# Kernel tuning notes

Hardware: AMD Instinct MI355X
Metric: run time of the kernel (lower is better)

Reference implementation:

```python
import jax, jax.numpy as jnp
import numpy as np

N_EMBED = 1024
N_HEAD = 16
HEAD_SIZE = N_EMBED // N_HEAD
LN_EPS = 1e-5


def setup_inputs() -> dict:
    key = jax.random.key(0)
    ks = jax.random.split(key, 12)
    B, T, C = 8, 1024, N_EMBED
    s = 0.02
    return {
        "x": jax.random.normal(ks[0], (B, T, C), dtype=jnp.float32),
        "Wq": jax.random.normal(ks[1], (C, C), dtype=jnp.float32) * s,
        "Wk": jax.random.normal(ks[2], (C, C), dtype=jnp.float32) * s,
        "Wv": jax.random.normal(ks[3], (C, C), dtype=jnp.float32) * s,
        "Wp": jax.random.normal(ks[4], (C, C), dtype=jnp.float32) * s,
        "bp": jnp.zeros((C,), dtype=jnp.float32),
        "ln1_g": jnp.ones((C,), dtype=jnp.float32),
        "ln1_b": jnp.zeros((C,), dtype=jnp.float32),
        "ln2_g": jnp.ones((C,), dtype=jnp.float32),
        "ln2_b": jnp.zeros((C,), dtype=jnp.float32),
        "W1": jax.random.normal(ks[5], (C, 4 * C), dtype=jnp.float32) * s,
        "b1": jnp.zeros((4 * C,), dtype=jnp.float32),
        "W2": jax.random.normal(ks[6], (4 * C, C), dtype=jnp.float32) * s,
        "b2": jnp.zeros((C,), dtype=jnp.float32),
    }


def _layernorm(x, g, b):
    mu = jnp.mean(x, axis=-1, keepdims=True)
    var = jnp.mean(jnp.square(x - mu), axis=-1, keepdims=True)
    return (x - mu) * jax.lax.rsqrt(var + LN_EPS) * g + b


def _block(x, Wq, Wk, Wv, Wp, bp, ln1_g, ln1_b, ln2_g, ln2_b, W1, b1, W2, b2):
    B, T, C = x.shape
    H, D = N_HEAD, HEAD_SIZE
    xn = _layernorm(x, ln1_g, ln1_b)
    # fused QKV for all heads (heads concatenated along feature dim, same as torch cat)
    q = (xn @ Wq).reshape(B, T, H, D)
    k = (xn @ Wk).reshape(B, T, H, D)
    v = (xn @ Wv).reshape(B, T, H, D)
    scores = jnp.einsum("bthd,bshd->bhts", q, k) / jnp.sqrt(jnp.float32(D))
    causal = jnp.tril(jnp.ones((T, T), dtype=bool))
    scores = jnp.where(causal, scores, jnp.float32(-jnp.inf))
    wei = jax.nn.softmax(scores, axis=-1)  # dropout = identity (eval)
    attn = jnp.einsum("bhts,bshd->bthd", wei, v).reshape(B, T, C)
    sa_out = attn @ Wp + bp  # dropout = identity (eval)
    x = x + sa_out
    xn2 = _layernorm(x, ln2_g, ln2_b)
    ff = jax.nn.relu(xn2 @ W1 + b1) @ W2 + b2  # dropout = identity (eval)
    return x + ff


def reference(x, Wq, Wk, Wv, Wp, bp, ln1_g, ln1_b, ln2_g, ln2_b, W1, b1, W2, b2):
    return _block(x, Wq, Wk, Wv, Wp, bp, ln1_g, ln1_b, ln2_g, ln2_b, W1, b1, W2, b2)
```

## Files before the change

kernel.cpp:

```cpp
#include <hip/hip_runtime.h>
#include <cstdint>
#include <cstddef>

using u16 = unsigned short;
typedef __attribute__((ext_vector_type(8))) short bh8;
typedef __attribute__((ext_vector_type(4))) float f4;

__device__ __forceinline__ u16 f2bf(float f) {
    union { float f; uint32_t u; } c; c.f = f;
    uint32_t u = c.u;
    u += 0x7FFFu + ((u >> 16) & 1u);
    return (u16)(u >> 16);
}

__device__ __forceinline__ void gload16(const void* g, void* l) {
    __builtin_amdgcn_global_load_lds(
        (__attribute__((address_space(1))) void*)g,
        (__attribute__((address_space(3))) void*)l,
        16, 0, 0);
}

__device__ __forceinline__ f4 mfma16(bh8 a, bh8 b, f4 c) {
    return __builtin_amdgcn_mfma_f32_16x16x32_bf16(a, b, c, 0, 0, 0);
}

__global__ __launch_bounds__(256) void wconv_kernel(
    const float* __restrict__ W, u16* __restrict__ Wt, int K, int N)
{
    __shared__ float t[32][33];
    const int tx = threadIdx.x & 31, ty = threadIdx.x >> 5;
    const int n0 = blockIdx.x * 32, k0 = blockIdx.y * 32;
#pragma unroll
    for (int j = 0; j < 4; ++j)
        t[ty + 8 * j][tx] = W[(size_t)(k0 + ty + 8 * j) * N + n0 + tx];
    __syncthreads();
#pragma unroll
    for (int j = 0; j < 4; ++j)
        Wt[(size_t)(n0 + ty + 8 * j) * K + k0 + tx] = f2bf(t[tx][ty + 8 * j]);
}

__global__ __launch_bounds__(256) void ln_kernel(
    const float* __restrict__ x, const float* __restrict__ g,
    const float* __restrict__ b, u16* __restrict__ out)
{
    const int row = blockIdx.x;
    const int tid = threadIdx.x;
    const float4 v = ((const float4*)(x + (size_t)row * 1024))[tid];
    float s  = v.x + v.y + v.z + v.w;
    float sq = v.x * v.x + v.y * v.y + v.z * v.z + v.w * v.w;
#pragma unroll
    for (int m = 1; m < 64; m <<= 1) {
        s  += __shfl_xor(s, m);
        sq += __shfl_xor(sq, m);
    }
    __shared__ float red[8];
    const int w = tid >> 6;
    if ((tid & 63) == 0) { red[w * 2] = s; red[w * 2 + 1] = sq; }
    __syncthreads();
    s  = red[0] + red[2] + red[4] + red[6];
    sq = red[1] + red[3] + red[5] + red[7];
    const float mu   = s * (1.0f / 1024.0f);
    const float var  = sq * (1.0f / 1024.0f) - mu * mu;
    const float rstd = rsqrtf(var + 1e-5f);
    const float4 gv = ((const float4*)g)[tid];
    const float4 bv = ((const float4*)b)[tid];
    ushort4 o;
    o.x = f2bf((v.x - mu) * rstd * gv.x + bv.x);
    o.y = f2bf((v.y - mu) * rstd * gv.y + bv.y);
    o.z = f2bf((v.z - mu) * rstd * gv.z + bv.z);
    o.w = f2bf((v.w - mu) * rstd * gv.w + bv.w);
    ((ushort4*)(out + (size_t)row * 1024))[tid] = o;
}

__global__ __launch_bounds__(256) void vtrans_kernel(
    const u16* __restrict__ vb, u16* __restrict__ vtb)
{
    __shared__ u16 t[64][66];
    const int bh = blockIdx.y;
    const int t0 = blockIdx.x * 64;
    const int b = bh >> 4, h = bh & 15;
    const u16* src = vb + (size_t)b * 1024 * 1024 + h * 64;
    const int rs = threadIdx.x >> 3, cs = threadIdx.x & 7;
#pragma unroll
    for (int it = 0; it < 2; ++it) {
        const int r = it * 32 + rs;
        *(uint4*)&t[r][cs * 8] = *(const uint4*)(src + (size_t)(t0 + r) * 1024 + cs * 8);
    }
    __syncthreads();
    u16* dst = vtb + (size_t)bh * 65536 + t0;
#pragma unroll
    for (int it = 0; it < 2; ++it) {
        const int d = it * 32 + rs;
        u16 tmp[8];
#pragma unroll
        for (int j = 0; j < 8; ++j) tmp[j] = t[cs * 8 + j][d];
        *(uint4*)(dst + (size_t)d * 1024 + cs * 8) = *(const uint4*)tmp;
    }
}

template <int NF, int EPI>
__global__ __launch_bounds__(512) void gemm8_kernel(
    const u16* __restrict__ A, const u16* __restrict__ Bt,
    int M, int N, int K, int KT,
    const float* __restrict__ bias, const float* __restrict__ resid,
    float* __restrict__ outf, u16* __restrict__ outb)
{
    constexpr int BN = NF * 64;
    __shared__ u16 Al[2][256 * 64];
    __shared__ u16 Bl[2][BN * 64];

    const int tid  = threadIdx.x;
    const int lane = tid & 63;
    const int w    = tid >> 6;
    const int wr   = w >> 2;
    const int wc   = w & 3;
    const int lrow = lane & 15;
    const int lg   = lane >> 4;

    const int gx  = gridDim.x, gy = gridDim.y;
    const int nwg = gx * gy * gridDim.z;
    const int lin = (blockIdx.z * gy + blockIdx.y) * gx + blockIdx.x;
    const int swz = (lin & 7) * (nwg >> 3) + (lin >> 3);
    const int nt  = swz % gx;
    const int tmq = swz / gx;
    const int mt  = tmq % gy;
    const int kz  = tmq / gy;
    const int kb  = kz * KT;

    auto stageA = [&](int slot, int h, int kt) {
#pragma unroll
        for (int it = 0; it < 2; ++it) {
            const int r = h * 128 + it * 64 + (tid >> 3);
            gload16(A + (size_t)(mt * 256 + r) * K + kt * 64 + (((tid & 7) ^ (r & 7)) << 3),
                    (char*)Al[slot] + (h * 128 + it * 64) * 128 + tid * 16);
        }
    };
    auto stageB = [&](int slot, int h, int kt) {
#pragma unroll
        for (int it = 0; it < NF / 2; ++it) {
            const int r = h * (BN / 2) + it * 64 + (tid >> 3);
            gload16(Bt + (size_t)(nt * BN + r) * K + kt * 64 + (((tid & 7) ^ (r & 7)) << 3),
                    (char*)Bl[slot] + (h * (BN / 2) + it * 64) * 128 + tid * 16);
        }
    };

    f4 acc[8][NF] = {};
    bh8 af[8];
    bh8 bf[NF];

    auto readFrags = [&](int slot, int ks) {
#pragma unroll
        for (int fm = 0; fm < 8; ++fm) {
            const int R = wr * 128 + fm * 16 + lrow;
            af[fm] = *(const bh8*)&Al[slot][R * 64 + ((((ks << 2) + lg) ^ (R & 7)) << 3)];
        }
#pragma unroll
        for (int fn = 0; fn < NF; ++fn) {
            const int R = wc * (NF * 16) + fn * 16 + lrow;
            bf[fn] = *(const bh8*)&Bl[slot][R * 64 + ((((ks << 2) + lg) ^ (R & 7)) << 3)];
        }
    };
    auto mfmaHalf = [&](int mh) {
#pragma unroll
        for (int fm = 0; fm < 4; ++fm)
#pragma unroll
            for (int fn = 0; fn < NF; ++fn)
                acc[mh * 4 + fm][fn] = mfma16(af[mh * 4 + fm], bf[fn], acc[mh * 4 + fm][fn]);
    };

    stageA(0, 0, kb); stageA(0, 1, kb); stageB(0, 0, kb); stageB(0, 1, kb);
    stageA(1, 0, kb + 1);
    asm volatile("s_waitcnt vmcnt(2)" ::: "memory");
    __builtin_amdgcn_s_barrier();
    __builtin_amdgcn_sched_barrier(0);

    auto doTile = [&](int t, int s, bool stN, bool stN2, bool g2) {
        readFrags(s, 0);
        if (stN) stageA(s ^ 1, 1, kb + t + 1);
        __builtin_amdgcn_s_barrier();
        asm volatile("s_waitcnt lgkmcnt(0)" ::: "memory");
        __builtin_amdgcn_sched_barrier(0);
        __builtin_amdgcn_s_setprio(1);
        mfmaHalf(0);
        __builtin_amdgcn_s_setprio(0);
        __builtin_amdgcn_s_barrier();
        __builtin_amdgcn_sched_barrier(0);
        if (stN) stageB(s ^ 1, 0, kb + t + 1);
        __builtin_amdgcn_s_barrier();
        __builtin_amdgcn_sched_barrier(0);
        __builtin_amdgcn_s_setprio(1);
        mfmaHalf(1);
        __builtin_amdgcn_s_setprio(0);
        __builtin_amdgcn_s_barrier();
        __builtin_amdgcn_sched_barrier(0);
        readFrags(s, 1);
        if (stN) stageB(s ^ 1, 1, kb + t + 1);
        __builtin_amdgcn_s_barrier();
        asm volatile("s_waitcnt lgkmcnt(0)" ::: "memory");
        __builtin_amdgcn_sched_barrier(0);
        __builtin_amdgcn_s_setprio(1);
        mfmaHalf(0);
        __builtin_amdgcn_s_setprio(0);
        __builtin_amdgcn_s_barrier();
        __builtin_amdgcn_sched_barrier(0);
        if (stN2) stageA(s, 0, kb + t + 2);
        __builtin_amdgcn_s_barrier();
        __builtin_amdgcn_sched_barrier(0);
        __builtin_amdgcn_s_setprio(1);
        mfmaHalf(1);
        __builtin_amdgcn_s_setprio(0);
        if (g2) asm volatile("s_waitcnt vmcnt(2)" ::: "memory");
        else    asm volatile("s_waitcnt vmcnt(0)" ::: "memory");
        __builtin_amdgcn_s_barrier();
        __builtin_amdgcn_sched_barrier(0);
    };

    for (int t = 0; t < KT - 2; t += 2) {
        doTile(t,     0, true, true, true);
        doTile(t + 1, 1, true, true, true);
    }
    doTile(KT - 2, 0, true,  false, false);
    doTile(KT - 1, 1, false, false, false);

    const int r0 = mt * 256 + wr * 128 + lg * 4;
    const int c0 = nt * BN + wc * (NF * 16) + lrow;
#pragma unroll
    for (int fn = 0; fn < NF; ++fn) {
        const int col = c0 + fn * 16;
        float bvl = 0.0f;
        if (EPI == 1 || EPI == 2) bvl = bias[col];
        if (EPI == 4 && kz == 0)  bvl = bias[col];
#pragma unroll
        for (int fm = 0; fm < 8; ++fm) {
#pragma unroll
            for (int i = 0; i < 4; ++i) {
                const int rr = r0 + fm * 16 + i;
                const float v = acc[fm][fn][i];
                if (EPI == 1) {
                    const size_t idx = (size_t)rr * N + col;
                    outf[idx] = resid[idx] + v + bvl;
                } else if (EPI == 2) {
                    outb[(size_t)rr * N + col] = f2bf(fmaxf(v + bvl, 0.0f));
                } else if (EPI == 3) {
                    outb[(size_t)(col >> 10) * 8388608 + (size_t)rr * 1024 + (col & 1023)]
                        = f2bf(v);
                } else {
                    atomicAdd(&outf[(size_t)rr * N + col], v + bvl);
                }
            }
        }
    }
}

__global__ __launch_bounds__(256, 3) void attn_kernel(
    const u16* __restrict__ Q, const u16* __restrict__ K,
    const u16* __restrict__ Vt, u16* __restrict__ O)
{
    __shared__ u16 Kl[2][64 * 64];
    __shared__ u16 Vl[2][64 * 64];
    __shared__ u16 Pl[4][16 * 72];

    const int tid  = threadIdx.x;
    const int lane = tid & 63;
    const int w    = tid >> 6;
    const int bh   = blockIdx.y;
    const size_t base  = (size_t)(bh >> 4) * (1024 * 1024) + (bh & 15) * 64;
    const size_t vbase = (size_t)bh * 65536;
    const int lrow = lane & 15;
    const int lg   = lane >> 4;
    const int lkb  = lg * 8;
    const int rs   = tid >> 3, cs = tid & 7;

    const u16* Kp = K + base;
    const u16* Vp = Vt + vbase;

#pragma unroll 1
    for (int p = 0; p < 2; ++p) {
        const int qt = p ? (15 - blockIdx.x) : blockIdx.x;
        const int q0 = qt * 64;

        const bh8 aq0 = *(const bh8*)(Q + base + (size_t)(q0 + w * 16 + lrow) * 1024 + lkb);
        const bh8 aq1 = *(const bh8*)(Q + base + (size_t)(q0 + w * 16 + lrow) * 1024 + 32 + lkb);

        f4 o[4] = {};
        float mi[4], li[4];
#pragma unroll
        for (int i = 0; i < 4; ++i) { mi[i] = -__builtin_inff(); li[i] = 0.0f; }

#pragma unroll
        for (int it = 0; it < 2; ++it) {
            const int r = it * 32 + rs;
            gload16(Kp + (size_t)r * 1024 + ((cs ^ (r & 7)) * 8),
                    (char*)Kl[0] + it * 4096 + tid * 16);
            gload16(Vp + (size_t)r * 1024 + ((cs ^ (r & 7)) * 8),
                    (char*)Vl[0] + it * 4096 + tid * 16);
        }
        __syncthreads();

        for (int t = 0; t <= qt; ++t) {
            const int cur = t & 1;
            if (t < qt) {
                const int s1 = (t + 1) * 64;
#pragma unroll
                for (int it = 0; it < 2; ++it) {
                    const int r = it * 32 + rs;
                    gload16(Kp + (size_t)(s1 + r) * 1024 + ((cs ^ (r & 7)) * 8),
                            (char*)Kl[cur ^ 1] + it * 4096 + tid * 16);
                    gload16(Vp + (size_t)r * 1024 + s1 + ((cs ^ (r & 7)) * 8),
                            (char*)Vl[cur ^ 1] + it * 4096 + tid * 16);
                }
            }

            f4 sc[4] = {};
#pragma unroll
            for (int ks = 0; ks < 2; ++ks) {
                const bh8 a = ks ? aq1 : aq0;
#pragma unroll
                for (int fn = 0; fn < 4; ++fn) {
                    const int R = fn * 16 + lrow;
                    const bh8 bk = *(const bh8*)&Kl[cur][R * 64 + ((((ks << 2) + lg) ^ (R & 7)) * 8)];
                    sc[fn] = mfma16(a, bk, sc[fn]);
                }
            }
            const bool diag = (t == qt);
#pragma unroll
            for (int fn = 0; fn < 4; ++fn)
#pragma unroll
                for (int i = 0; i < 4; ++i) {
                    float v = sc[fn][i] * 0.125f;
                    if (diag) {
                        const int r = lg * 4 + i;
                        const int c = fn * 16 + lrow;
                        if (c > w * 16 + r) v = -__builtin_inff();
                    }
                    sc[fn][i] = v;
                }
#pragma unroll
            for (int i = 0; i < 4; ++i) {
                float pm = fmaxf(fmaxf(sc[0][i], sc[1][i]), fmaxf(sc[2][i], sc[3][i]));
#pragma unroll
                for (int m = 1; m < 16; m <<= 1) pm = fmaxf(pm, __shfl_xor(pm, m));
                const float mn   = fmaxf(mi[i], pm);
                const float corr = __expf(mi[i] - mn);
                float rsum = 0.0f;
#pragma unroll
                for (int fn = 0; fn < 4; ++fn) {
                    const float pv = __expf(sc[fn][i] - mn);
                    sc[fn][i] = pv;
                    rsum += pv;
                }
#pragma unroll
                for (int m = 1; m < 16; m <<= 1) rsum += __shfl_xor(rsum, m);
                li[i] = li[i] * corr + rsum;
                mi[i] = mn;
#pragma unroll
                for (int fn = 0; fn < 4; ++fn) o[fn][i] *= corr;
            }
#pragma unroll
            for (int fn = 0; fn < 4; ++fn)
#pragma unroll
                for (int i = 0; i < 4; ++i)
                    Pl[w][(lg * 4 + i) * 72 + fn * 16 + lrow] = f2bf(sc[fn][i]);
#pragma unroll
            for (int ss = 0; ss < 2; ++ss) {
                const bh8 ap = *(const bh8*)&Pl[w][lrow * 72 + ss * 32 + lkb];
#pragma unroll
                for (int fn = 0; fn < 4; ++fn) {
                    const int R = fn * 16 + lrow;
                    const bh8 bv = *(const bh8*)&Vl[cur][R * 64 + ((((ss << 2) + lg) ^ (R & 7)) * 8)];
                    o[fn] = mfma16(ap, bv, o[fn]);
                }
            }
            __syncthreads();
        }

#pragma unroll
        for (int fn = 0; fn < 4; ++fn)
#pragma unroll
            for (int i = 0; i < 4; ++i) {
                const int r = q0 + w * 16 + lg * 4 + i;
                const int c = fn * 16 + lrow;
                O[base + (size_t)r * 1024 + c] = f2bf(o[fn][i] / li[i]);
            }
    }
}

extern "C" void kernel_launch(void* const* d_in, const int* in_sizes, int n_in,
                              void* d_out, int out_size, void* d_ws, size_t ws_size,
                              hipStream_t stream) {
    const float* x    = (const float*)d_in[0];
    const float* Wq   = (const float*)d_in[1];
    const float* Wk   = (const float*)d_in[2];
    const float* Wv   = (const float*)d_in[3];
    const float* Wp   = (const float*)d_in[4];
    const float* bp   = (const float*)d_in[5];
    const float* ln1g = (const float*)d_in[6];
    const float* ln1b = (const float*)d_in[7];
    const float* ln2g = (const float*)d_in[8];
    const float* ln2b = (const float*)d_in[9];
    const float* W1   = (const float*)d_in[10];
    const float* b1   = (const float*)d_in[11];
    const float* W2   = (const float*)d_in[12];
    const float* b2   = (const float*)d_in[13];
    float* out = (float*)d_out;

    u16* ws   = (u16*)d_ws;
    u16* wqkt = ws;
    u16* wpt  = wqkt + (3u << 20);
    u16* w1t  = wpt  + (1u << 20);
    u16* w2t  = w1t  + (4u << 20);
    u16* qb   = w2t  + (4u << 20);
    u16* kb   = qb   + (8u << 20);
    u16* vb   = kb   + (8u << 20);
    u16* xnb  = vb   + (8u << 20);
    u16* vtb  = xnb;
    u16* aob  = vb;
    u16* xn2b = qb;
    u16* h1b  = kb;

    dim3 blk(256);
    wconv_kernel<<<dim3(32, 32),  blk, 0, stream>>>(Wq, wqkt,              1024, 1024);
    wconv_kernel<<<dim3(32, 32),  blk, 0, stream>>>(Wk, wqkt + (1u << 20), 1024, 1024);
    wconv_kernel<<<dim3(32, 32),  blk, 0, stream>>>(Wv, wqkt + (2u << 20), 1024, 1024);
    wconv_kernel<<<dim3(32, 32),  blk, 0, stream>>>(Wp, wpt, 1024, 1024);
    wconv_kernel<<<dim3(128, 32), blk, 0, stream>>>(W1, w1t, 1024, 4096);
    wconv_kernel<<<dim3(32, 128), blk, 0, stream>>>(W2, w2t, 4096, 1024);

    ln_kernel<<<8192, blk, 0, stream>>>(x, ln1g, ln1b, xnb);

    gemm8_kernel<4, 3><<<dim3(12, 32, 1), 512, 0, stream>>>(
        xnb, wqkt, 8192, 3072, 1024, 16, nullptr, nullptr, nullptr, qb);

    vtrans_kernel<<<dim3(16, 128), blk, 0, stream>>>(vb, vtb);

    attn_kernel<<<dim3(8, 128), blk, 0, stream>>>(qb, kb, vtb, aob);

    gemm8_kernel<2, 1><<<dim3(8, 32, 1), 512, 0, stream>>>(
        aob, wpt, 8192, 1024, 1024, 16, bp, x, out, nullptr);

    ln_kernel<<<8192, blk, 0, stream>>>(out, ln2g, ln2b, xn2b);

    gemm8_kernel<4, 2><<<dim3(16, 32, 1), 512, 0, stream>>>(
        xn2b, w1t, 8192, 4096, 1024, 16, b1, nullptr, nullptr, h1b);

    gemm8_kernel<4, 4><<<dim3(4, 32, 2), 512, 0, stream>>>(
        h1b, w2t, 8192, 1024, 4096, 32, b2, nullptr, out, nullptr);
}
```

Before: 403.3 us.

## Split GEMM LDS tiles into K-halves and restructure the load/MFMA pipeline

Shared-memory A/B tiles are split into two 32-wide K halves per slot, with a new XOR swizzle suited to 64-byte rows. The main loop now interleaves staging of each K-half with four quarter-step MFMA phases and waits on finer vmcnt gates. A fragments are read per M-half, so only four A fragments stay live, which lowers register pressure. The aim is finer-grained overlap of global-to-LDS loads with compute. The risk is more barriers per tile, and the new swizzle may change LDS bank conflicts.

```diff
diff --git a/kernel.cpp b/kernel.cpp
--- a/kernel.cpp
+++ b/kernel.cpp
@@ -106,8 +106,8 @@
     float* __restrict__ outf, u16* __restrict__ outb)
 {
     constexpr int BN = NF * 64;
-    __shared__ u16 Al[2][256 * 64];
-    __shared__ u16 Bl[2][BN * 64];
+    __shared__ u16 Al[2][2][256 * 32];
+    __shared__ u16 Bl[2][2][BN * 32];
 
     const int tid  = threadIdx.x;
     const int lane = tid & 63;
@@ -127,92 +127,89 @@
     const int kz  = tmq / gy;
     const int kb  = kz * KT;
 
-    auto stageA = [&](int slot, int h, int kt) {
+    auto stageA = [&](int slot, int ks, int kt) {
 #pragma unroll
         for (int it = 0; it < 2; ++it) {
-            const int r = h * 128 + it * 64 + (tid >> 3);
-            gload16(A + (size_t)(mt * 256 + r) * K + kt * 64 + (((tid & 7) ^ (r & 7)) << 3),
-                    (char*)Al[slot] + (h * 128 + it * 64) * 128 + tid * 16);
-        }
-    };
-    auto stageB = [&](int slot, int h, int kt) {
-#pragma unroll
-        for (int it = 0; it < NF / 2; ++it) {
-            const int r = h * (BN / 2) + it * 64 + (tid >> 3);
-            gload16(Bt + (size_t)(nt * BN + r) * K + kt * 64 + (((tid & 7) ^ (r & 7)) << 3),
-                    (char*)Bl[slot] + (h * (BN / 2) + it * 64) * 128 + tid * 16);
+            const int r = it * 128 + (tid >> 2);
+            gload16(A + (size_t)(mt * 256 + r) * K + kt * 64 + ks * 32
+                        + (((tid & 3) ^ ((r >> 1) & 3)) << 3),
+                    (char*)&Al[slot][ks][0] + it * 8192 + tid * 16);
+        }
+    };
+    auto stageB = [&](int slot, int ks, int kt) {
+#pragma unroll
+        for (int it = 0; it < BN / 128; ++it) {
+            const int r = it * 128 + (tid >> 2);
+            gload16(Bt + (size_t)(nt * BN + r) * K + kt * 64 + ks * 32
+                         + (((tid & 3) ^ ((r >> 1) & 3)) << 3),
+                    (char*)&Bl[slot][ks][0] + it * 8192 + tid * 16);
         }
     };
 
     f4 acc[8][NF] = {};
-    bh8 af[8];
+    bh8 af[4];
     bh8 bf[NF];
 
-    auto readFrags = [&](int slot, int ks) {
-#pragma unroll
-        for (int fm = 0; fm < 8; ++fm) {
-            const int R = wr * 128 + fm * 16 + lrow;
-            af[fm] = *(const bh8*)&Al[slot][R * 64 + ((((ks << 2) + lg) ^ (R & 7)) << 3)];
-        }
+    auto readA = [&](int slot, int ks, int mh) {
+#pragma unroll
+        for (int fm = 0; fm < 4; ++fm) {
+            const int R = wr * 128 + mh * 64 + fm * 16 + lrow;
+            af[fm] = *(const bh8*)&Al[slot][ks][R * 32 + ((lg ^ ((R >> 1) & 3)) << 3)];
+        }
+    };
+    auto readB = [&](int slot, int ks) {
 #pragma unroll
         for (int fn = 0; fn < NF; ++fn) {
             const int R = wc * (NF * 16) + fn * 16 + lrow;
-            bf[fn] = *(const bh8*)&Bl[slot][R * 64 + ((((ks << 2) + lg) ^ (R & 7)) << 3)];
-        }
-    };
-    auto mfmaHalf = [&](int mh) {
+            bf[fn] = *(const bh8*)&Bl[slot][ks][R * 32 + ((lg ^ ((R >> 1) & 3)) << 3)];
+        }
+    };
+    auto mfmaQ = [&](int mh) {
 #pragma unroll
         for (int fm = 0; fm < 4; ++fm)
 #pragma unroll
             for (int fn = 0; fn < NF; ++fn)
-                acc[mh * 4 + fm][fn] = mfma16(af[mh * 4 + fm], bf[fn], acc[mh * 4 + fm][fn]);
-    };
-
-    stageA(0, 0, kb); stageA(0, 1, kb); stageB(0, 0, kb); stageB(0, 1, kb);
-    stageA(1, 0, kb + 1);
-    asm volatile("s_waitcnt vmcnt(2)" ::: "memory");
-    __builtin_amdgcn_s_barrier();
-    __builtin_amdgcn_sched_barrier(0);
-
-    auto doTile = [&](int t, int s, bool stN, bool stN2, bool g2) {
-        readFrags(s, 0);
-        if (stN) stageA(s ^ 1, 1, kb + t + 1);
+                acc[mh * 4 + fm][fn] = mfma16(af[fm], bf[fn], acc[mh * 4 + fm][fn]);
+    };
+
+    auto syncMid = [&]() {
         __builtin_amdgcn_s_barrier();
         asm volatile("s_waitcnt lgkmcnt(0)" ::: "memory");
         __builtin_amdgcn_sched_barrier(0);
         __builtin_amdgcn_s_setprio(1);
-        mfmaHalf(0);
+    };
+    auto syncEnd = [&](int gate) {
         __builtin_amdgcn_s_setprio(0);
+        if (gate == 1) {
+            if constexpr (NF == 4) asm volatile("s_waitcnt vmcnt(8)" ::: "memory");
+            else                   asm volatile("s_waitcnt vmcnt(6)" ::: "memory");
+        } else if (gate == 2) {
+            asm volatile("s_waitcnt vmcnt(0)" ::: "memory");
+        }
         __builtin_amdgcn_s_barrier();
         __builtin_amdgcn_sched_barrier(0);
-        if (stN) stageB(s ^ 1, 0, kb + t + 1);
-        __builtin_amdgcn_s_barrier();
-        __builtin_amdgcn_sched_barrier(0);
-        __builtin_amdgcn_s_setprio(1);
-        mfmaHalf(1);
-        __builtin_amdgcn_s_setprio(0);
-        __builtin_amdgcn_s_barrier();
-        __builtin_amdgcn_sched_barrier(0);
-        readFrags(s, 1);
-        if (stN) stageB(s ^ 1, 1, kb + t + 1);
-        __builtin_amdgcn_s_barrier();
-        asm volatile("s_waitcnt lgkmcnt(0)" ::: "memory");
-        __builtin_amdgcn_sched_barrier(0);
-        __builtin_amdgcn_s_setprio(1);
-        mfmaHalf(0);
-        __builtin_amdgcn_s_setprio(0);
-        __builtin_amdgcn_s_barrier();
-        __builtin_amdgcn_sched_barrier(0);
-        if (stN2) stageA(s, 0, kb + t + 2);
-        __builtin_amdgcn_s_barrier();
-        __builtin_amdgcn_sched_barrier(0);
-        __builtin_amdgcn_s_setprio(1);
-        mfmaHalf(1);
-        __builtin_amdgcn_s_setprio(0);
-        if (g2) asm volatile("s_waitcnt vmcnt(2)" ::: "memory");
-        else    asm volatile("s_waitcnt vmcnt(0)" ::: "memory");
-        __builtin_amdgcn_s_barrier();
-        __builtin_amdgcn_sched_barrier(0);
+    };
+
+    stageA(0, 0, kb); stageB(0, 0, kb); stageA(0, 1, kb); stageB(0, 1, kb);
+    stageA(1, 0, kb + 1); stageB(1, 0, kb + 1);
+    if constexpr (NF == 4) asm volatile("s_waitcnt vmcnt(4)" ::: "memory");
+    else                   asm volatile("s_waitcnt vmcnt(3)" ::: "memory");
+    __builtin_amdgcn_s_barrier();
+    __builtin_amdgcn_sched_barrier(0);
+
+    auto doTile = [&](int t, int s, bool st1, bool st2, bool g) {
+        readA(s, 0, 0); readB(s, 0);
+        if (st1) stageA(s ^ 1, 1, kb + t + 1);
+        syncMid(); mfmaQ(0); syncEnd(0);
+        readA(s, 0, 1);
+        if (st1) stageB(s ^ 1, 1, kb + t + 1);
+        syncMid(); mfmaQ(1); syncEnd(g ? 1 : 2);
+        readA(s, 1, 0); readB(s, 1);
+        if (st2) stageA(s, 0, kb + t + 2);
+        syncMid(); mfmaQ(0); syncEnd(0);
+        readA(s, 1, 1);
+        if (st2) stageB(s, 0, kb + t + 2);
+        syncMid(); mfmaQ(1); syncEnd(g ? 1 : 2);
     };
 
     for (int t = 0; t < KT - 2; t += 2) {
```

New measurement: 412.3 us. 1.02x slower.
